# Optimization experiments

Measured on AMD Instinct MI355X. Metric: run time of the kernel, lower is better.

## Reference

```python
import jax, jax.numpy as jnp
import numpy as np

DMODEL = 1024
N_EXPERTS = 16
EXPERT_SIZE = 256
K = 4


def setup_inputs() -> dict:
    key = jax.random.key(0)
    k1, k2, k3, k4 = jax.random.split(key, 4)
    std_sel = 1.0 / np.sqrt(DMODEL)
    std_val = 1.0 / np.sqrt(N_EXPERTS * EXPERT_SIZE)
    return {
        "x": jax.random.normal(k1, (4, 2048, DMODEL), dtype=jnp.float32),
        "expert_sel": jax.random.normal(k2, (N_EXPERTS, DMODEL), dtype=jnp.float32) * std_sel,
        "keys": jax.random.normal(k3, (N_EXPERTS, DMODEL, EXPERT_SIZE), dtype=jnp.float32) * std_sel,
        "values": jax.random.normal(k4, (N_EXPERTS, EXPERT_SIZE, DMODEL), dtype=jnp.float32) * std_val,
        "route_scale": jnp.ones((1,), dtype=jnp.float32),
    }


def reference(x, expert_sel, keys, values, route_scale):
    # Routing: sigmoid gating, top-k selection (eval mode: no dropout/bias balancing)
    sel_logits = jnp.einsum("btd,ed->bte", x, expert_sel)  # [B,T,E]
    sel_probs = jax.nn.sigmoid(sel_logits)
    _, sel_index = jax.lax.top_k(sel_probs, K)  # [B,T,K]
    sel_val = jnp.take_along_axis(sel_probs, sel_index, axis=-1)  # [B,T,K]
    sel_val = sel_val / jnp.clip(sel_val.sum(-1, keepdims=True), 1e-9)
    sel_val = sel_val * route_scale  # route_scale shape [1] broadcasts
    # Dense all-expert FFN (as in original), then gather top-k and combine
    scores_all = jax.nn.relu(jnp.einsum("btd,edh->bteh", x, keys))  # [B,T,E,H]
    values_all = jnp.einsum("bteh,ehv->btev", scores_all, values)   # [B,T,E,V]
    sel_idx_exp = sel_index[..., None]  # [B,T,K,1]
    selected = jnp.take_along_axis(values_all, sel_idx_exp, axis=2)  # [B,T,K,V]
    out = (selected * sel_val[..., None]).sum(axis=2)  # [B,T,V]
    return out
```

## Files before the change

### kernel.cpp

```cpp
#include <hip/hip_runtime.h>
#include <math.h>


constexpr int NTOK = 8192;
constexpr int DM   = 1024;
constexpr int NE   = 16;
constexpr int EH   = 256;
constexpr int TK   = 4;
constexpr int CAP  = 8192;

typedef __attribute__((ext_vector_type(8))) short short8;
typedef __attribute__((ext_vector_type(4))) float f32x4;

#define MFMA16(a, b, c) __builtin_amdgcn_mfma_f32_16x16x32_bf16(a, b, c, 0, 0, 0)

__device__ __forceinline__ void gload_lds16(const void* g, void* l) {
    __builtin_amdgcn_global_load_lds(
        (const __attribute__((address_space(1))) void*)g,
        (__attribute__((address_space(3))) void*)l, 16, 0, 0);
}

__device__ __forceinline__ unsigned short f2bf(float f) {
    union { float f; unsigned int u; } x; x.f = f;
    unsigned int r = x.u + 0x7fffu + ((x.u >> 16) & 1u);
    return (unsigned short)(r >> 16);
}
__device__ __forceinline__ float bf2f(unsigned short b) {
    union { unsigned int u; float f; } x; x.u = ((unsigned int)b) << 16;
    return x.f;
}

__global__ __launch_bounds__(256) void route_conv_kernel(
    const float* __restrict__ x, const float* __restrict__ esel,
    const float* __restrict__ rscale,
    unsigned short* __restrict__ xb,
    int4* __restrict__ sel4, float* __restrict__ wtk)
{
    __shared__ float Es[NE * DM];
    int tid = threadIdx.x;

    {
        const float4* src = (const float4*)esel;
        float4* dst = (float4*)Es;
        #pragma unroll
        for (int j = 0; j < 16; ++j) dst[tid + j * 256] = src[tid + j * 256];
    }
    __syncthreads();

    int t    = blockIdx.x * 8 + (tid >> 5);
    int l32  = tid & 31;

    float acc[NE];
    #pragma unroll
    for (int e = 0; e < NE; ++e) acc[e] = 0.f;

    const float4* x4 = (const float4*)(x + (size_t)t * DM);
    const float4* E4 = (const float4*)Es;
    #pragma unroll
    for (int i4 = 0; i4 < 8; ++i4) {
        int d4 = i4 * 32 + l32;
        float4 xv = x4[d4];
        ushort4 cb = { f2bf(xv.x), f2bf(xv.y), f2bf(xv.z), f2bf(xv.w) };
        *(ushort4*)(xb + (size_t)t * DM + d4 * 4) = cb;
        #pragma unroll
        for (int e = 0; e < NE; ++e) {
            float4 wv = E4[e * 256 + d4];
            acc[e] = fmaf(xv.x, wv.x, acc[e]);
            acc[e] = fmaf(xv.y, wv.y, acc[e]);
            acc[e] = fmaf(xv.z, wv.z, acc[e]);
            acc[e] = fmaf(xv.w, wv.w, acc[e]);
        }
    }

    #pragma unroll
    for (int off = 16; off; off >>= 1)
        #pragma unroll
        for (int e = 0; e < NE; ++e)
            acc[e] += __shfl_xor(acc[e], off, 32);

    if (l32 == 0) {
        float p[NE];
        #pragma unroll
        for (int e = 0; e < NE; ++e) p[e] = 1.0f / (1.0f + expf(-acc[e]));

        int   sel_e[TK];
        float sel_p[TK];
        float sum = 0.f;
        #pragma unroll
        for (int k = 0; k < TK; ++k) {
            float best = -INFINITY; int be = NE;
            #pragma unroll
            for (int e = 0; e < NE; ++e) {
                bool take = p[e] > best;
                best = take ? p[e] : best;
                be   = take ? e    : be;
            }
            sel_e[k] = be; sel_p[k] = best; sum += best;
            #pragma unroll
            for (int e = 0; e < NE; ++e) p[e] = (e == be) ? -INFINITY : p[e];
        }

        float wsc = rscale[0] / fmaxf(sum, 1e-9f);
        int4 s = { sel_e[0], sel_e[1], sel_e[2], sel_e[3] };
        sel4[t] = s;
        float4 wv = { sel_p[0] * wsc, sel_p[1] * wsc,
                      sel_p[2] * wsc, sel_p[3] * wsc };
        *(float4*)(wtk + t * TK) = wv;
    }
}

__global__ __launch_bounds__(1024) void compact_kernel(
    const int4* __restrict__ sel4, int* __restrict__ counts,
    int* __restrict__ lpk)
{
    __shared__ int wsum[16];
    int e    = blockIdx.x;
    int tid  = threadIdx.x;
    int w    = tid >> 6;
    int lane = tid & 63;

    int base = 0;
    for (int c = 0; c < NTOK; c += 1024) {
        int t = c + tid;
        int4 s = sel4[t];
        int k = -1;
        if      (s.x == e) k = 0;
        else if (s.y == e) k = 1;
        else if (s.z == e) k = 2;
        else if (s.w == e) k = 3;
        unsigned long long m = __ballot(k >= 0);
        int rank = __popcll(m & ((1ull << lane) - 1ull));
        if (lane == 63) wsum[w] = __popcll(m);
        __syncthreads();
        int prefix = 0, total = 0;
        #pragma unroll
        for (int i = 0; i < 16; ++i) {
            int v = wsum[i];
            prefix += (i < w) ? v : 0;
            total  += v;
        }
        if (k >= 0) lpk[e * CAP + base + prefix + rank] = t * TK + k;
        base += total;
        __syncthreads();
    }
    if (tid == 0) counts[e] = base;
}

__global__ __launch_bounds__(256) void trans_kernel(
    const float* __restrict__ in, unsigned short* __restrict__ outp, int R, int C)
{
    __shared__ float T[32][33];
    int e = blockIdx.z;
    int r0 = blockIdx.y * 32, c0 = blockIdx.x * 32;
    int ri = threadIdx.x >> 3, cq = threadIdx.x & 7;
    float4 v = *(const float4*)(in + ((size_t)e * R + r0 + ri) * C + c0 + cq * 4);
    T[ri][cq * 4 + 0] = v.x; T[ri][cq * 4 + 1] = v.y;
    T[ri][cq * 4 + 2] = v.z; T[ri][cq * 4 + 3] = v.w;
    __syncthreads();
    int ci = threadIdx.x >> 3, rq = threadIdx.x & 7;
    ushort4 o = { f2bf(T[rq * 4 + 0][ci]), f2bf(T[rq * 4 + 1][ci]),
                  f2bf(T[rq * 4 + 2][ci]), f2bf(T[rq * 4 + 3][ci]) };
    *(ushort4*)(outp + ((size_t)e * C + c0 + ci) * R + r0 + rq * 4) = o;
}

__global__ __launch_bounds__(256) void transV_kernel(
    const float* __restrict__ in, unsigned short* __restrict__ outp)
{
    __shared__ float T[64][33];
    int e  = blockIdx.z;
    int c0 = blockIdx.x * 32;
    int r0 = blockIdx.y * 64;
    int tid = threadIdx.x;
    int kin = tid >> 3, cq = tid & 7;
    {
        float4 v0 = *(const float4*)(in + ((size_t)e * EH + r0 + kin) * DM + c0 + cq * 4);
        float4 v1 = *(const float4*)(in + ((size_t)e * EH + r0 + kin + 32) * DM + c0 + cq * 4);
        T[kin][cq * 4 + 0] = v0.x; T[kin][cq * 4 + 1] = v0.y;
        T[kin][cq * 4 + 2] = v0.z; T[kin][cq * 4 + 3] = v0.w;
        T[kin + 32][cq * 4 + 0] = v1.x; T[kin + 32][cq * 4 + 1] = v1.y;
        T[kin + 32][cq * 4 + 2] = v1.z; T[kin + 32][cq * 4 + 3] = v1.w;
    }
    __syncthreads();
    #pragma unroll
    for (int uu = 0; uu < 2; ++uu) {
        int u = tid + uu * 256;
        int d = u >> 4, lm = u & 15;
        ushort4 o = { f2bf(T[lm][d]), f2bf(T[lm + 16][d]),
                      f2bf(T[lm + 32][d]), f2bf(T[lm + 48][d]) };
        *(ushort4*)(outp + (size_t)e * DM * EH + (size_t)(c0 + d) * EH + r0 + lm * 4) = o;
    }
}

__global__ __launch_bounds__(256, 4) void gemm1_kernel(
    const unsigned short* __restrict__ xb,
    const unsigned short* __restrict__ ktb,
    const int* __restrict__ counts, const int* __restrict__ lpk,
    unsigned short* __restrict__ S)
{
    __shared__ __align__(16) char L[25088];
    char* const Ab = L;
    char* const Bb = L + 16384;
    int* const stok = (int*)(L + 24576);

    int tid = threadIdx.x, lane = tid & 63, w = tid >> 6;
    int lm = lane & 15, q = lane >> 4;

    int xp = blockIdx.x & 7, j0 = blockIdx.x >> 3;
    int e0 = xp * 2;
    int c0n = counts[e0], c1n = counts[e0 + 1];
    int n0 = (c0n + 127) >> 7, n1 = (c1n + 127) >> 7;
    int ntot = (n0 + n1) * 4;
    int gb0 = 0;
    for (int i = 0; i < e0; ++i) gb0 += ((counts[i] + 127) >> 7) << 7;
    int gb1 = gb0 + (n0 << 7);

    for (int jt = j0; jt < ntot; jt += 128) {
        int e, mt, nt, cnt, gb;
        if (jt < n0 * 4) { e = e0;     mt = jt >> 2;  nt = jt & 3;  cnt = c0n; gb = gb0; }
        else { int j2 = jt - n0 * 4; e = e0 + 1; mt = j2 >> 2; nt = j2 & 3; cnt = c1n; gb = gb1; }

        __syncthreads();
        if (tid < 128) {
            int s = mt * 128 + tid;
            stok[tid] = (s < cnt) ? (lpk[e * CAP + s] >> 2) : 0;
        }
        __syncthreads();

        const unsigned short* kte = ktb + (size_t)e * EH * DM + (size_t)(nt * 64) * DM;

        f32x4 zero = {0.f, 0.f, 0.f, 0.f};
        f32x4 acc[2][4];
        #pragma unroll
        for (int mi = 0; mi < 2; ++mi)
            #pragma unroll
            for (int ni = 0; ni < 4; ++ni) acc[mi][ni] = zero;

        for (int ks = 0; ks < 16; ++ks) {
            if (ks) __syncthreads();
            #pragma unroll
            for (int c = 0; c < 4; ++c) {
                int pos = c * 4096 + w * 1024;
                int row = (pos >> 7) + (lane >> 3);
                int ce  = (((lane & 7) * 16) ^ ((row & 7) << 4)) >> 1;
                gload_lds16(xb + (size_t)stok[row] * DM + ks * 64 + ce, Ab + pos);
            }
            #pragma unroll
            for (int c = 0; c < 2; ++c) {
                int pos = c * 4096 + w * 1024;
                int row = (pos >> 7) + (lane >> 3);
                int ce  = (((lane & 7) * 16) ^ ((row & 7) << 4)) >> 1;
                gload_lds16(kte + (size_t)row * DM + ks * 64 + ce, Bb + pos);
            }
            __syncthreads();
            #pragma unroll
            for (int kk = 0; kk < 2; ++kk) {
                short8 a[2], b[4];
                #pragma unroll
                for (int mi = 0; mi < 2; ++mi) {
                    int row = w * 32 + mi * 16 + lm;
                    a[mi] = *(const short8*)(Ab + row * 128 +
                             ((kk * 64 + q * 16) ^ ((row & 7) << 4)));
                }
                #pragma unroll
                for (int ni = 0; ni < 4; ++ni) {
                    int row = ni * 16 + lm;
                    b[ni] = *(const short8*)(Bb + row * 128 +
                             ((kk * 64 + q * 16) ^ ((row & 7) << 4)));
                }
                __builtin_amdgcn_s_setprio(1);
                #pragma unroll
                for (int mi = 0; mi < 2; ++mi)
                    #pragma unroll
                    for (int ni = 0; ni < 4; ++ni)
                        acc[mi][ni] = MFMA16(a[mi], b[ni], acc[mi][ni]);
                __builtin_amdgcn_s_setprio(0);
            }
        }

        #pragma unroll
        for (int mi = 0; mi < 2; ++mi)
            #pragma unroll
            for (int r = 0; r < 4; ++r) {
                int gslot = gb + mt * 128 + w * 32 + mi * 16 + q * 4 + r;
                unsigned int lo = (unsigned int)f2bf(fmaxf(acc[mi][0][r], 0.f)) |
                                  ((unsigned int)f2bf(fmaxf(acc[mi][1][r], 0.f)) << 16);
                unsigned int hi = (unsigned int)f2bf(fmaxf(acc[mi][2][r], 0.f)) |
                                  ((unsigned int)f2bf(fmaxf(acc[mi][3][r], 0.f)) << 16);
                uint2 pv = { lo, hi };
                *(uint2*)(S + (size_t)gslot * EH + nt * 64 + lm * 4) = pv;
            }
    }
}

template<int USE_SCRATCH>
__global__ __launch_bounds__(256, 4) void gemm2_kernel(
    const unsigned short* __restrict__ S,
    const unsigned short* __restrict__ vtb,
    const int* __restrict__ counts, const int* __restrict__ lpk,
    const float* __restrict__ wtk,
    unsigned short* __restrict__ oscr,
    float* __restrict__ out)
{
    __shared__ __align__(16) char L[25344];
    char* const Ab = L;
    char* const Bb = L + 8192;
    int*   const spk  = (int*)(L + 24576);
    int*   const stok = (int*)(L + 24832);
    float* const sw   = (float*)(L + 25088);

    int tid = threadIdx.x, lane = tid & 63, w = tid >> 6;
    int lm = lane & 15, q = lane >> 4;
    int wm = w >> 1, wn = w & 1;

    int xp = blockIdx.x & 7, j0 = blockIdx.x >> 3;
    int e0 = xp * 2;
    int c0n = counts[e0], c1n = counts[e0 + 1];
    int m0 = (c0n + 63) >> 6, m1 = (c1n + 63) >> 6;
    int ntot = (m0 + m1) * 8;
    int gb0 = 0;
    for (int i = 0; i < e0; ++i) gb0 += ((counts[i] + 127) >> 7) << 7;
    int gb1 = gb0 + (((c0n + 127) >> 7) << 7);

    for (int jt = j0; jt < ntot; jt += 512) {
        int e, mt, nt, cnt, gb;
        if (jt < m0 * 8) { e = e0;     mt = jt >> 3;  nt = jt & 7;  cnt = c0n; gb = gb0; }
        else { int j2 = jt - m0 * 8; e = e0 + 1; mt = j2 >> 3; nt = j2 & 7; cnt = c1n; gb = gb1; }

        __syncthreads();
        if (tid < 64) {
            int s = mt * 64 + tid;
            if (s < cnt) {
                int pk = lpk[e * CAP + s];
                spk[tid] = pk;
                if (!USE_SCRATCH) { stok[tid] = pk >> 2; sw[tid] = wtk[pk]; }
            } else {
                spk[tid] = NTOK * TK;
                if (!USE_SCRATCH) { stok[tid] = 0; sw[tid] = 0.f; }
            }
        }
        __syncthreads();

        const unsigned short* Se  = S + (size_t)(gb + mt * 64) * EH;
        const unsigned short* vte = vtb + (size_t)e * DM * EH + (size_t)(nt * 128) * EH;

        f32x4 zero = {0.f, 0.f, 0.f, 0.f};
        f32x4 acc[2][4];
        #pragma unroll
        for (int mi = 0; mi < 2; ++mi)
            #pragma unroll
            for (int ni = 0; ni < 4; ++ni) acc[mi][ni] = zero;

        #pragma unroll
        for (int ks = 0; ks < 4; ++ks) {
            if (ks) __syncthreads();
            #pragma unroll
            for (int c = 0; c < 2; ++c) {
                int pos = c * 4096 + w * 1024;
                int row = (pos >> 7) + (lane >> 3);
                int ce  = (((lane & 7) * 16) ^ ((row & 7) << 4)) >> 1;
                gload_lds16(Se + (size_t)row * EH + ks * 64 + ce, Ab + pos);
            }
            #pragma unroll
            for (int c = 0; c < 4; ++c) {
                int pos = c * 4096 + w * 1024;
                int row = (pos >> 7) + (lane >> 3);
                int ce  = (((lane & 7) * 16) ^ ((row & 7) << 4)) >> 1;
                gload_lds16(vte + (size_t)row * EH + ks * 64 + ce, Bb + pos);
            }
            __syncthreads();
            #pragma unroll
            for (int kk = 0; kk < 2; ++kk) {
                short8 a[2], b[4];
                #pragma unroll
                for (int mi = 0; mi < 2; ++mi) {
                    int row = wm * 32 + mi * 16 + lm;
                    a[mi] = *(const short8*)(Ab + row * 128 +
                             ((kk * 64 + q * 16) ^ ((row & 7) << 4)));
                }
                #pragma unroll
                for (int ni = 0; ni < 4; ++ni) {
                    int row = wn * 64 + ni * 16 + lm;
                    b[ni] = *(const short8*)(Bb + row * 128 +
                             ((kk * 64 + q * 16) ^ ((row & 7) << 4)));
                }
                __builtin_amdgcn_s_setprio(1);
                #pragma unroll
                for (int mi = 0; mi < 2; ++mi)
                    #pragma unroll
                    for (int ni = 0; ni < 4; ++ni)
                        acc[mi][ni] = MFMA16(a[mi], b[ni], acc[mi][ni]);
                __builtin_amdgcn_s_setprio(0);
            }
        }

        int cb64 = nt * 2 + wn;
        #pragma unroll
        for (int mi = 0; mi < 2; ++mi)
            #pragma unroll
            for (int r = 0; r < 4; ++r) {
                int slot = wm * 32 + mi * 16 + q * 4 + r;
                if (USE_SCRATCH) {
                    int pk = spk[slot];
                    unsigned int lo = (unsigned int)f2bf(acc[mi][0][r]) |
                                      ((unsigned int)f2bf(acc[mi][1][r]) << 16);
                    unsigned int hi = (unsigned int)f2bf(acc[mi][2][r]) |
                                      ((unsigned int)f2bf(acc[mi][3][r]) << 16);
                    uint2 pv = { lo, hi };
                    *(uint2*)(oscr + (size_t)pk * DM + cb64 * 64 + lm * 4) = pv;
                } else {
                    #pragma unroll
                    for (int ni = 0; ni < 4; ++ni) {
                        int d = cb64 * 64 + ni * 16 + lm;
                        atomicAdd(out + (size_t)stok[slot] * DM + d,
                                  sw[slot] * acc[mi][ni][r]);
                    }
                }
            }
    }
}

__global__ __launch_bounds__(256) void combine_kernel(
    const unsigned short* __restrict__ oscr, const float* __restrict__ wtk,
    float* __restrict__ out)
{
    int t   = blockIdx.x * 2 + (threadIdx.x >> 7);
    int l   = threadIdx.x & 127;
    int blk = l >> 3;
    int lm2 = l & 7;
    float o[8] = {0.f, 0.f, 0.f, 0.f, 0.f, 0.f, 0.f, 0.f};
    #pragma unroll
    for (int k = 0; k < TK; ++k) {
        float wv = wtk[t * TK + k];
        uint4 qv = *(const uint4*)(oscr + (size_t)(t * TK + k) * DM +
                                   blk * 64 + lm2 * 8);
        unsigned int us[4] = { qv.x, qv.y, qv.z, qv.w };
        #pragma unroll
        for (int j = 0; j < 4; ++j) {
            o[j * 2 + 0] = fmaf(wv, bf2f((unsigned short)(us[j] & 0xffff)), o[j * 2 + 0]);
            o[j * 2 + 1] = fmaf(wv, bf2f((unsigned short)(us[j] >> 16)),    o[j * 2 + 1]);
        }
    }
    float* ob = out + (size_t)t * DM + blk * 64 + 2 * lm2;
    #pragma unroll
    for (int ni = 0; ni < 4; ++ni) {
        float2 f2 = { o[ni], o[ni + 4] };
        *(float2*)(ob + ni * 16) = f2;
    }
}

extern "C" void kernel_launch(void* const* d_in, const int* in_sizes, int n_in,
                              void* d_out, int out_size, void* d_ws, size_t ws_size,
                              hipStream_t stream) {
    const float* x      = (const float*)d_in[0];
    const float* esel   = (const float*)d_in[1];
    const float* keys   = (const float*)d_in[2];
    const float* values = (const float*)d_in[3];
    const float* rscale = (const float*)d_in[4];
    float* out = (float*)d_out;

    char* ws = (char*)d_ws;
    size_t o = 0;
    auto alloc = [&](size_t sz) { size_t r = o; o = (o + sz + 255) & ~(size_t)255; return r; };
    size_t o_counts = alloc(NE * 4);
    size_t o_lpk    = alloc((size_t)NE * CAP * 4);
    size_t o_sel4   = alloc((size_t)NTOK * 16);
    size_t o_wtk    = alloc((size_t)NTOK * TK * 4);
    size_t o_xb     = alloc((size_t)NTOK * DM * 2);
    size_t o_ktb    = alloc((size_t)NE * EH * DM * 2);
    size_t o_vtb    = alloc((size_t)NE * DM * EH * 2);
    size_t o_S      = alloc(((size_t)NTOK * TK + NE * 128) * EH * 2);
    size_t need_small = o;
    size_t o_oscr   = alloc(((size_t)NTOK * TK + 128) * DM * 2);
    size_t need_full = o;

    int*            counts = (int*)(ws + o_counts);
    int*            lpk    = (int*)(ws + o_lpk);
    int4*           sel4   = (int4*)(ws + o_sel4);
    float*          wtk    = (float*)(ws + o_wtk);
    unsigned short* xb     = (unsigned short*)(ws + o_xb);
    unsigned short* ktb    = (unsigned short*)(ws + o_ktb);
    unsigned short* vtb    = (unsigned short*)(ws + o_vtb);
    unsigned short* Sbuf   = (unsigned short*)(ws + o_S);
    unsigned short* oscr   = (unsigned short*)(ws + o_oscr);

    bool use_scratch = ws_size >= need_full;
    (void)need_small;

    if (!use_scratch)
        hipMemsetAsync(d_out, 0, (size_t)out_size * sizeof(float), stream);

    route_conv_kernel<<<NTOK / 8, 256, 0, stream>>>(x, esel, rscale, xb,
                                                    sel4, wtk);
    compact_kernel<<<NE, 1024, 0, stream>>>(sel4, counts, lpk);
    trans_kernel<<<dim3(EH / 32, DM / 32, NE), 256, 0, stream>>>(keys, ktb, DM, EH);
    transV_kernel<<<dim3(DM / 32, EH / 64, NE), 256, 0, stream>>>(values, vtb);

    gemm1_kernel<<<1024, 256, 0, stream>>>(xb, ktb, counts, lpk, Sbuf);

    if (use_scratch) {
        gemm2_kernel<1><<<4096, 256, 0, stream>>>(Sbuf, vtb, counts,
                                                  lpk, wtk, oscr, out);
        combine_kernel<<<NTOK / 2, 256, 0, stream>>>(oscr, wtk, out);
    } else {
        gemm2_kernel<0><<<4096, 256, 0, stream>>>(Sbuf, vtb, counts,
                                                  lpk, wtk, oscr, out);
    }
}
```

Baseline: 123.4 us.

## Keep full A tile resident in LDS and double-buffer V across all N tiles

Each gemm2 block now loads its entire 64x256 slice of S once into LDS and loops over all eight 128-column N tiles, streaming V^T tiles through a double-buffered LDS region so the next stage's load overlaps the current MFMA work. This removes the eightfold reload of the A tile and the load/compute serialization, but uses about 66 KB of LDS, so occupancy drops to two blocks and the grid shrinks from 4096 to 512 blocks, which could hurt load balance across CUs.

```diff
diff --git a/kernel.cpp b/kernel.cpp
--- a/kernel.cpp
+++ b/kernel.cpp
@@ -293,7 +293,7 @@
 }
 
 template<int USE_SCRATCH>
-__global__ __launch_bounds__(256, 4) void gemm2_kernel(
+__global__ __launch_bounds__(256, 2) void gemm2_kernel(
     const unsigned short* __restrict__ S,
     const unsigned short* __restrict__ vtb,
     const int* __restrict__ counts, const int* __restrict__ lpk,
@@ -301,12 +301,12 @@
     unsigned short* __restrict__ oscr,
     float* __restrict__ out)
 {
-    __shared__ __align__(16) char L[25344];
+    __shared__ __align__(16) char L[32768 + 32768 + 768];
     char* const Ab = L;
-    char* const Bb = L + 8192;
-    int*   const spk  = (int*)(L + 24576);
-    int*   const stok = (int*)(L + 24832);
-    float* const sw   = (float*)(L + 25088);
+    char* const Bb = L + 32768;
+    int*   const spk  = (int*)(L + 65536);
+    int*   const stok = (int*)(L + 65536 + 256);
+    float* const sw   = (float*)(L + 65536 + 512);
 
     int tid = threadIdx.x, lane = tid & 63, w = tid >> 6;
     int lm = lane & 15, q = lane >> 4;
@@ -316,15 +316,15 @@
     int e0 = xp * 2;
     int c0n = counts[e0], c1n = counts[e0 + 1];
     int m0 = (c0n + 63) >> 6, m1 = (c1n + 63) >> 6;
-    int ntot = (m0 + m1) * 8;
+    int ntot = m0 + m1;
     int gb0 = 0;
     for (int i = 0; i < e0; ++i) gb0 += ((counts[i] + 127) >> 7) << 7;
     int gb1 = gb0 + (((c0n + 127) >> 7) << 7);
 
-    for (int jt = j0; jt < ntot; jt += 512) {
-        int e, mt, nt, cnt, gb;
-        if (jt < m0 * 8) { e = e0;     mt = jt >> 3;  nt = jt & 7;  cnt = c0n; gb = gb0; }
-        else { int j2 = jt - m0 * 8; e = e0 + 1; mt = j2 >> 3; nt = j2 & 7; cnt = c1n; gb = gb1; }
+    for (int jt = j0; jt < ntot; jt += 64) {
+        int e, mt, cnt, gb;
+        if (jt < m0) { e = e0;     mt = jt;      cnt = c0n; gb = gb0; }
+        else         { e = e0 + 1; mt = jt - m0; cnt = c1n; gb = gb1; }
 
         __syncthreads();
         if (tid < 64) {
@@ -338,49 +338,63 @@
                 if (!USE_SCRATCH) { stok[tid] = 0; sw[tid] = 0.f; }
             }
         }
-        __syncthreads();
 
         const unsigned short* Se  = S + (size_t)(gb + mt * 64) * EH;
-        const unsigned short* vte = vtb + (size_t)e * DM * EH + (size_t)(nt * 128) * EH;
-
-        f32x4 zero = {0.f, 0.f, 0.f, 0.f};
-        f32x4 acc[2][4];
-        #pragma unroll
-        for (int mi = 0; mi < 2; ++mi)
-            #pragma unroll
-            for (int ni = 0; ni < 4; ++ni) acc[mi][ni] = zero;
-
-        #pragma unroll
-        for (int ks = 0; ks < 4; ++ks) {
-            if (ks) __syncthreads();
-            #pragma unroll
-            for (int c = 0; c < 2; ++c) {
-                int pos = c * 4096 + w * 1024;
-                int row = (pos >> 7) + (lane >> 3);
-                int ce  = (((lane & 7) * 16) ^ ((row & 7) << 4)) >> 1;
-                gload_lds16(Se + (size_t)row * EH + ks * 64 + ce, Ab + pos);
-            }
+        const unsigned short* vte = vtb + (size_t)e * DM * EH;
+
+        #pragma unroll
+        for (int it = 0; it < 8; ++it) {
+            int pos  = it * 4096 + tid * 16;
+            int row  = pos >> 9;
+            int colb = pos & 511;
+            int ce   = (colb ^ ((row & 7) << 4)) >> 1;
+            gload_lds16(Se + (size_t)row * EH + ce, Ab + pos);
+        }
+
+        auto stageB = [&](int u) {
+            int nt = u >> 2, ks = u & 3, buf = u & 1;
+            const unsigned short* src = vte + (size_t)(nt * 128) * EH + ks * 64;
+            char* dst = Bb + buf * 16384;
             #pragma unroll
             for (int c = 0; c < 4; ++c) {
                 int pos = c * 4096 + w * 1024;
                 int row = (pos >> 7) + (lane >> 3);
                 int ce  = (((lane & 7) * 16) ^ ((row & 7) << 4)) >> 1;
-                gload_lds16(vte + (size_t)row * EH + ks * 64 + ce, Bb + pos);
-            }
-            __syncthreads();
+                gload_lds16(src + (size_t)row * EH + ce, dst + pos);
+            }
+        };
+
+        stageB(0);
+        __syncthreads();
+
+        f32x4 zero = {0.f, 0.f, 0.f, 0.f};
+        f32x4 acc[2][4];
+
+        #pragma unroll 4
+        for (int u = 0; u < 32; ++u) {
+            int nt = u >> 2, ks = u & 3, buf = u & 1;
+            if (u) __syncthreads();
+            if (u < 31) stageB(u + 1);
+            if (ks == 0) {
+                #pragma unroll
+                for (int mi = 0; mi < 2; ++mi)
+                    #pragma unroll
+                    for (int ni = 0; ni < 4; ++ni) acc[mi][ni] = zero;
+            }
+            const char* Vb = Bb + buf * 16384;
             #pragma unroll
             for (int kk = 0; kk < 2; ++kk) {
                 short8 a[2], b[4];
                 #pragma unroll
                 for (int mi = 0; mi < 2; ++mi) {
                     int row = wm * 32 + mi * 16 + lm;
-                    a[mi] = *(const short8*)(Ab + row * 128 +
-                             ((kk * 64 + q * 16) ^ ((row & 7) << 4)));
+                    a[mi] = *(const short8*)(Ab + row * 512 +
+                             ((ks * 128 + kk * 64 + q * 16) ^ ((row & 7) << 4)));
                 }
                 #pragma unroll
                 for (int ni = 0; ni < 4; ++ni) {
                     int row = wn * 64 + ni * 16 + lm;
-                    b[ni] = *(const short8*)(Bb + row * 128 +
+                    b[ni] = *(const short8*)(Vb + row * 128 +
                              ((kk * 64 + q * 16) ^ ((row & 7) << 4)));
                 }
                 __builtin_amdgcn_s_setprio(1);
@@ -391,31 +405,32 @@
                         acc[mi][ni] = MFMA16(a[mi], b[ni], acc[mi][ni]);
                 __builtin_amdgcn_s_setprio(0);
             }
-        }
-
-        int cb64 = nt * 2 + wn;
-        #pragma unroll
-        for (int mi = 0; mi < 2; ++mi)
-            #pragma unroll
-            for (int r = 0; r < 4; ++r) {
-                int slot = wm * 32 + mi * 16 + q * 4 + r;
-                if (USE_SCRATCH) {
-                    int pk = spk[slot];
-                    unsigned int lo = (unsigned int)f2bf(acc[mi][0][r]) |
-                                      ((unsigned int)f2bf(acc[mi][1][r]) << 16);
-                    unsigned int hi = (unsigned int)f2bf(acc[mi][2][r]) |
-                                      ((unsigned int)f2bf(acc[mi][3][r]) << 16);
-                    uint2 pv = { lo, hi };
-                    *(uint2*)(oscr + (size_t)pk * DM + cb64 * 64 + lm * 4) = pv;
-                } else {
+            if (ks == 3) {
+                int cb64 = nt * 2 + wn;
+                #pragma unroll
+                for (int mi = 0; mi < 2; ++mi)
                     #pragma unroll
-                    for (int ni = 0; ni < 4; ++ni) {
-                        int d = cb64 * 64 + ni * 16 + lm;
-                        atomicAdd(out + (size_t)stok[slot] * DM + d,
-                                  sw[slot] * acc[mi][ni][r]);
+                    for (int r = 0; r < 4; ++r) {
+                        int slot = wm * 32 + mi * 16 + q * 4 + r;
+                        if (USE_SCRATCH) {
+                            int pk = spk[slot];
+                            unsigned int lo = (unsigned int)f2bf(acc[mi][0][r]) |
+                                              ((unsigned int)f2bf(acc[mi][1][r]) << 16);
+                            unsigned int hi = (unsigned int)f2bf(acc[mi][2][r]) |
+                                              ((unsigned int)f2bf(acc[mi][3][r]) << 16);
+                            uint2 pv = { lo, hi };
+                            *(uint2*)(oscr + (size_t)pk * DM + cb64 * 64 + lm * 4) = pv;
+                        } else {
+                            #pragma unroll
+                            for (int ni = 0; ni < 4; ++ni) {
+                                int d = cb64 * 64 + ni * 16 + lm;
+                                atomicAdd(out + (size_t)stok[slot] * DM + d,
+                                          sw[slot] * acc[mi][ni][r]);
+                            }
+                        }
                     }
-                }
-            }
+            }
+        }
     }
 }
 
@@ -498,11 +513,11 @@
     gemm1_kernel<<<1024, 256, 0, stream>>>(xb, ktb, counts, lpk, Sbuf);
 
     if (use_scratch) {
-        gemm2_kernel<1><<<4096, 256, 0, stream>>>(Sbuf, vtb, counts,
-                                                  lpk, wtk, oscr, out);
+        gemm2_kernel<1><<<512, 256, 0, stream>>>(Sbuf, vtb, counts,
+                                                 lpk, wtk, oscr, out);
         combine_kernel<<<NTOK / 2, 256, 0, stream>>>(oscr, wtk, out);
     } else {
-        gemm2_kernel<0><<<4096, 256, 0, stream>>>(Sbuf, vtb, counts,
-                                                  lpk, wtk, oscr, out);
-    }
-}
+        gemm2_kernel<0><<<512, 256, 0, stream>>>(Sbuf, vtb, counts,
+                                                 lpk, wtk, oscr, out);
+    }
+}
```

Result: slower. 134.1 us (+8.6%).
